# Kernel optimization log

Measured on AMD Instinct MI355X. Metric: run time of the kernel, lower is better.

Reference implementation:

```python
import jax, jax.numpy as jnp
import numpy as np
from jax import lax

# ---- static config (mirrors cfg) ----
ACT_SIZE = 768
GROUP_SIZES = [2048, 2048, 4096, 8192, 16384]
DICT_SIZE = sum(GROUP_SIZES)            # 32768
GROUP_IDX = np.concatenate([[0], np.cumsum(GROUP_SIZES)]).tolist()
TOP_K = 32
TOP_K_AUX = 512
L1_COEFF = 0.0003
AUX_PENALTY = 0.03125
N_DEAD = 5.0
THRESH_LR = 0.01
BATCH = 2048


def setup_inputs() -> dict:
    key = jax.random.key(0)
    k1, k2, k3, k4 = jax.random.split(key, 4)
    x = jax.random.normal(k1, (BATCH, ACT_SIZE), dtype=jnp.float32)
    W_enc = jax.random.normal(k2, (ACT_SIZE, DICT_SIZE), dtype=jnp.float32) * 0.02
    W_dec = jax.random.normal(k3, (DICT_SIZE, ACT_SIZE), dtype=jnp.float32)
    W_dec = W_dec / jnp.linalg.norm(W_dec, axis=-1, keepdims=True)  # unit-norm rows as in __init__
    num_batches_not_active = jax.random.randint(k4, (DICT_SIZE,), 0, 10).astype(jnp.float32)
    threshold = jnp.float32(0.0)
    return {"x": x, "W_enc": W_enc, "W_dec": W_dec, "b_dec": jnp.zeros((ACT_SIZE,), jnp.float32),
            "num_batches_not_active": num_batches_not_active, "threshold": threshold}


def reference(x, W_enc, W_dec, b_dec, num_batches_not_active, threshold):
    B, D = x.shape[0], DICT_SIZE
    # ---- preprocess (input_unit_norm=True) ----
    x_mean = x.mean(axis=-1, keepdims=True)
    x_std = jnp.std(x, axis=-1, keepdims=True, ddof=1)  # torch .std is unbiased
    xn = (x - x_mean) / (x_std + 1e-5)

    x_cent = xn - b_dec
    # ---- encode + global batch top-k (training path) ----
    acts = jax.nn.relu(x_cent @ W_enc)                  # [B, D]
    flat = acts.reshape(-1)
    k = TOP_K * B
    vals, idx = lax.top_k(flat, k)
    acts_topk = jnp.zeros_like(flat).at[idx].set(vals).reshape(B, D)

    # threshold EMA update (no_grad in torch)
    atk = lax.stop_gradient(acts_topk)
    pos = atk > 0
    min_pos = jnp.min(jnp.where(pos, atk, jnp.inf))
    new_threshold = jnp.where(pos.any(), (1 - THRESH_LR) * threshold + THRESH_LR * min_pos, threshold)

    # ---- matryoshka group decode ----
    x_reconstruct = jnp.broadcast_to(b_dec, xn.shape)
    inters = []
    for i in range(len(GROUP_SIZES)):
        s, e = GROUP_IDX[i], GROUP_IDX[i + 1]
        x_reconstruct = acts_topk[:, s:e] @ W_dec[s:e, :] + x_reconstruct
        inters.append(x_reconstruct)

    # ---- inactive-feature bookkeeping (no_grad) ----
    col_sums = lax.stop_gradient(acts_topk).sum(axis=0)
    nb = jnp.where(col_sums > 0, 0.0, num_batches_not_active + 1.0)

    # ---- loss dict ----
    total_l2 = jnp.mean((b_dec - xn) ** 2)
    l2s = jnp.stack([jnp.mean((r - xn) ** 2) for r in inters])
    total_l2 = total_l2 + l2s.sum()
    mean_l2 = total_l2 / (len(inters) + 1)
    x_var = jnp.var(xn, ddof=1)
    fvu = mean_l2 / (x_var + 1e-10)
    l1_norm = jnp.abs(acts_topk).sum(-1).mean()
    l0_norm = (acts_topk > 0).astype(jnp.float32).sum(-1).mean()
    l1_loss = L1_COEFF * l1_norm

    # ---- auxiliary loss over dead features ----
    dead = nb >= N_DEAD                                  # [D] bool, static count >> TOP_K_AUX here
    residual = xn - x_reconstruct
    masked = jnp.where(dead[None, :], acts, -jnp.inf)    # restrict top-k to dead features
    vals_a, idx_a = lax.top_k(masked, TOP_K_AUX)         # per-row top-k, [B, TOP_K_AUX]
    vals_a = jnp.where(jnp.isfinite(vals_a), vals_a, 0.0)
    acts_aux = jnp.zeros((B, D), acts.dtype).at[jnp.arange(B)[:, None], idx_a].set(vals_a)
    aux_reconstruct = acts_aux @ W_dec
    aux_mse = jnp.mean((aux_reconstruct - residual) ** 2)
    aux_loss = jnp.where(jnp.abs(aux_reconstruct).sum() > 0, AUX_PENALTY * aux_mse, 0.0)

    loss = mean_l2 + l1_loss + aux_loss
    num_dead_features = (nb > N_DEAD).sum()
    sae_out = x_reconstruct * x_std + x_mean

    return (sae_out, acts_topk, loss, l1_loss, mean_l2, l2s.min(), l2s.max(),
            l0_norm, l1_norm, aux_loss, new_threshold, fvu, num_dead_features)
```

## Files before the change

### kernel.cpp

```cpp
#include <hip/hip_runtime.h>
#include <stdint.h>

#define DEVFN static __device__ __forceinline__

typedef unsigned short u16;
typedef unsigned long long u64;
typedef short short8 __attribute__((ext_vector_type(8)));
typedef float vf4 __attribute__((ext_vector_type(4)));

constexpr int B = 2048;
constexpr int DIN = 768;
constexpr int D = 32768;
constexpr int NDI = B * D;
constexpr unsigned TOPK_TOTAL = 65536u;
constexpr int TOPK_AUX = 512;
constexpr int ROWCAP = 512;
constexpr int CANDCAP = 3145728;
constexpr int GSTAGE = 2048;
constexpr int CSTAGE = 4096;
constexpr int TIECAP = 4096;
constexpr int SCAP = 3072;
constexpr int NREP = 16;

constexpr size_t OFF_HIST1  = 0;
constexpr size_t OFF_HIST2  = 131072;
constexpr size_t OFF_HIST3  = 262144;
constexpr size_t OFF_HIST4  = 393216;
constexpr size_t OFF_SCALU  = 458752;
constexpr size_t OFF_SCALD  = 459008;
constexpr size_t OFF_ROWCNT = 459264;
constexpr size_t OFF_AUXCNT = 467456;
constexpr size_t OFF_COLACT = 475648;
constexpr size_t ZERO_BYTES = 606720;
constexpr size_t OFF_XN    = ZERO_BYTES;
constexpr size_t OFF_RES   = OFF_XN   + 6291456;
constexpr size_t OFF_RMEAN = OFF_RES  + 6291456;
constexpr size_t OFF_RSTD  = OFF_RMEAN + 8192;
constexpr size_t OFF_XNCB  = OFF_RSTD + 8192;
constexpr size_t OFF_DEAD  = OFF_XNCB + 3145728;
constexpr size_t OFF_DMASK = OFF_DEAD + 131072;
constexpr size_t OFF_DBASE = OFF_DMASK + 4096;
constexpr size_t OFF_RLC   = OFF_DBASE + 2048;
constexpr size_t OFF_RLV   = OFF_RLC  + 4194304;
constexpr size_t OFF_AXC   = OFF_RLV  + 4194304;
constexpr size_t OFF_AXV   = OFF_AXC  + 4194304;
constexpr size_t OFF_CANDI = OFF_AXV  + 4194304;
constexpr size_t OFF_CANDV = OFF_CANDI + (size_t)CANDCAP * 4;
constexpr size_t OFF_TIEB  = OFF_CANDV + (size_t)CANDCAP * 4;
constexpr size_t OFF_WT    = OFF_TIEB + (size_t)TIECAP * 4;


DEVFN u16 f2bf(float f) {
  unsigned u = __float_as_uint(f);
  unsigned r = (u + 0x7FFFu + ((u >> 16) & 1u)) >> 16;
  return (u16)r;
}
DEVFN float b2f(u16 h) { return __uint_as_float(((unsigned)h) << 16); }

DEVFN float bsumf(float v, float* red) {
  int t = threadIdx.x;
  red[t] = v; __syncthreads();
  for (int o = 128; o > 0; o >>= 1) { if (t < o) red[t] += red[t + o]; __syncthreads(); }
  float r = red[0]; __syncthreads();
  return r;
}
DEVFN unsigned bsumu(unsigned v, unsigned* red) {
  int t = threadIdx.x;
  red[t] = v; __syncthreads();
  for (int o = 128; o > 0; o >>= 1) { if (t < o) red[t] += red[t + o]; __syncthreads(); }
  unsigned r = red[0]; __syncthreads();
  return r;
}

DEVFN void findBin(const unsigned* hist, int nb, unsigned K, unsigned base,
                   unsigned* sscan, int* s_b, unsigned* s_cnt)
{
  int t = threadIdx.x;
  int chunk = nb >> 8;
  int hi = nb - 1 - t * chunk;
  unsigned p = 0;
  for (int k = 0; k < chunk; ++k) p += hist[hi - k];
  sscan[t] = p; __syncthreads();
  for (int o = 1; o < 256; o <<= 1) {
    unsigned xx = (t >= o) ? sscan[t - o] : 0u; __syncthreads();
    sscan[t] += xx; __syncthreads();
  }
  unsigned incl = sscan[t], excl = incl - p;
  unsigned cum = base + excl;
  if (base + incl >= K && cum < K) {
    unsigned acc = cum;
    for (int k = 0; k < chunk; ++k) {
      unsigned h = hist[hi - k];
      if (acc + h >= K) { *s_b = hi - k; *s_cnt = acc; break; }
      acc += h;
    }
  }
  __syncthreads();
}

__global__ __launch_bounds__(256) void k_rowstats(
    const float* __restrict__ x, const float* __restrict__ bdec,
    float* __restrict__ xn, u16* __restrict__ xncb,
    float* __restrict__ rmean, float* __restrict__ rstd, double* scalD)
{
  __shared__ float red[256];
  const int row = blockIdx.x, t = threadIdx.x;
  const float* xr = x + (size_t)row * DIN;
  float v0 = xr[t], v1 = xr[t + 256], v2 = xr[t + 512];
  float mean = bsumf(v0 + v1 + v2, red) * (1.0f / DIN);
  float d0 = v0 - mean, d1 = v1 - mean, d2 = v2 - mean;
  float var = bsumf(d0 * d0 + d1 * d1 + d2 * d2, red) * (1.0f / (DIN - 1));
  float sd = sqrtf(var);
  float inv = 1.0f / (sd + 1e-5f);
  float n0 = d0 * inv, n1 = d1 * inv, n2 = d2 * inv;
  size_t o = (size_t)row * DIN;
  xn[o + t] = n0; xn[o + t + 256] = n1; xn[o + t + 512] = n2;
  float b0 = bdec[t], b1 = bdec[t + 256], b2 = bdec[t + 512];
  xncb[o + t] = f2bf(n0 - b0); xncb[o + t + 256] = f2bf(n1 - b1); xncb[o + t + 512] = f2bf(n2 - b2);
  if (t == 0) { rmean[row] = mean; rstd[row] = sd; }
  float sxn = bsumf(n0 + n1 + n2, red);
  float ssq = bsumf(n0 * n0 + n1 * n1 + n2 * n2, red);
  float e0 = b0 - n0, e1 = b1 - n1, e2 = b2 - n2;
  float sq0 = bsumf(e0 * e0 + e1 * e1 + e2 * e2, red);
  if (t == 0) {
    atomicAdd(&scalD[1], (double)sxn);
    atomicAdd(&scalD[2], (double)ssq);
    atomicAdd(&scalD[3], (double)sq0);
  }
}

__global__ __launch_bounds__(256) void k_wt(const float* __restrict__ W, u16* __restrict__ Wt)
{
  __shared__ float tl[64][65];
  const int t = threadIdx.x;
  const int n0 = blockIdx.x * 64, k0 = blockIdx.y * 64;
  const int rr = t >> 6, cc = t & 63;
#pragma unroll
  for (int r = 0; r < 16; ++r) {
    int kk = r * 4 + rr;
    tl[kk][cc] = W[(size_t)(k0 + kk) * D + n0 + cc];
  }
  __syncthreads();
#pragma unroll
  for (int r = 0; r < 16; ++r) {
    int nn = r * 4 + rr;
    Wt[(size_t)(n0 + nn) * DIN + k0 + cc] = f2bf(tl[cc][nn]);
  }
}

__global__ __launch_bounds__(256) void k_wdecb(const float4* __restrict__ W4, u16* __restrict__ Wb)
{
  int stride = gridDim.x * blockDim.x;
  const int n4 = (D * DIN) / 4;
  for (int i = blockIdx.x * 256 + threadIdx.x; i < n4; i += stride) {
    float4 f = W4[i];
    unsigned p0 = (unsigned)f2bf(f.x) | ((unsigned)f2bf(f.y) << 16);
    unsigned p1 = (unsigned)f2bf(f.z) | ((unsigned)f2bf(f.w) << 16);
    uint2 q; q.x = p0; q.y = p1;
    *(uint2*)&Wb[(size_t)i * 4] = q;
  }
}

__global__ __launch_bounds__(256) void k_gemm(const u16* __restrict__ A,
                                              const u16* __restrict__ Bt,
                                              float* __restrict__ C,
                                              unsigned* __restrict__ hist16,
                                              unsigned* __restrict__ scalU,
                                              unsigned* __restrict__ candI,
                                              float* __restrict__ candV)
{
  __shared__ __align__(16) char lds[32768];
  __shared__ unsigned sCnt, sBase;
  const int tid = threadIdx.x, lane = tid & 63, wid = tid >> 6;
  const int bm = blockIdx.x * 128, bn = blockIdx.y * 128;

  const char* pA[4]; const char* pB[4];
#pragma unroll
  for (int i = 0; i < 4; ++i) {
    int G = i * 256 + wid * 64 + lane;
    int r = G >> 3, c = (G & 7) ^ (r & 7);
    pA[i] = (const char*)(A + (size_t)(bm + r) * DIN + c * 8);
    pB[i] = (const char*)(Bt + (size_t)(bn + r) * DIN + c * 8);
  }
  int aoff[2][4], boff[2][4];
#pragma unroll
  for (int kc = 0; kc < 2; ++kc)
#pragma unroll
    for (int i = 0; i < 4; ++i) {
      int cs = kc * 4 + (lane >> 4);
      int rA = (wid >> 1) * 64 + i * 16 + (lane & 15);
      aoff[kc][i] = rA * 128 + ((cs ^ (rA & 7)) * 16);
      int rB = (wid & 1) * 64 + i * 16 + (lane & 15);
      boff[kc][i] = 16384 + rB * 128 + ((cs ^ (rB & 7)) * 16);
    }

  vf4 acc[4][4];
#pragma unroll
  for (int i = 0; i < 4; ++i)
#pragma unroll
    for (int j = 0; j < 4; ++j) acc[i][j] = (vf4)0.f;

  for (int ks = 0; ks < 12; ++ks) {
    __syncthreads();
#pragma unroll
    for (int i = 0; i < 4; ++i) {
      __builtin_amdgcn_global_load_lds(
          (const __attribute__((address_space(1))) void*)pA[i],
          (__attribute__((address_space(3))) void*)(lds + (i * 256 + wid * 64) * 16), 16, 0, 0);
      __builtin_amdgcn_global_load_lds(
          (const __attribute__((address_space(1))) void*)pB[i],
          (__attribute__((address_space(3))) void*)(lds + 16384 + (i * 256 + wid * 64) * 16), 16, 0, 0);
      pA[i] += 128; pB[i] += 128;
    }
    __syncthreads();
#pragma unroll
    for (int kc = 0; kc < 2; ++kc) {
      short8 av[4], bv[4];
#pragma unroll
      for (int i = 0; i < 4; ++i) {
        av[i] = *(const short8*)(lds + aoff[kc][i]);
        bv[i] = *(const short8*)(lds + boff[kc][i]);
      }
#pragma unroll
      for (int i = 0; i < 4; ++i)
#pragma unroll
        for (int j = 0; j < 4; ++j)
          acc[i][j] = __builtin_amdgcn_mfma_f32_16x16x32_bf16(av[i], bv[j], acc[i][j], 0, 0, 0);
    }
  }

  unsigned* h = (unsigned*)lds;
  unsigned* stIdx = (unsigned*)(lds + 8192);
  float* stVal = (float*)(lds + 16384);
  __syncthreads();
  for (int j = tid; j < 2048; j += 256) h[j] = 0;
  if (tid == 0) sCnt = 0;
  __syncthreads();

  const int r0 = bm + (wid >> 1) * 64 + (lane >> 4) * 4;
  const int c0 = bn + (wid & 1) * 64 + (lane & 15);
#pragma unroll
  for (int i = 0; i < 4; ++i)
#pragma unroll
    for (int j = 0; j < 4; ++j) {
      float* cp = C + (size_t)(r0 + i * 16) * D + c0 + j * 16;
#pragma unroll
      for (int q = 0; q < 4; ++q) {
        float v = fmaxf(acc[i][j][q], 0.f);
        cp[(size_t)q * D] = v;
        if (v >= 1.0f) {
          atomicAdd(&h[__float_as_uint(v) >> 21], 1u);
          unsigned idx = ((unsigned)(r0 + i * 16 + q) << 15) | (unsigned)(c0 + j * 16);
          unsigned p = atomicAdd(&sCnt, 1u);
          if (p < (unsigned)GSTAGE) { stIdx[p] = idx; stVal[p] = v; }
          else {
            unsigned g = atomicAdd(&scalU[12], 1u);
            if (g < (unsigned)CANDCAP) { candI[g] = idx; candV[g] = v; }
          }
        }
      }
    }
  __syncthreads();
  unsigned* dst = hist16 + (size_t)(blockIdx.x & (NREP - 1)) * 2048;
  for (int j = 508 + tid; j < 2048; j += 256) {
    unsigned c = h[j];
    if (c) atomicAdd(&dst[j], c);
  }
  unsigned n = sCnt < (unsigned)GSTAGE ? sCnt : (unsigned)GSTAGE;
  if (tid == 0) sBase = atomicAdd(&scalU[12], n);
  __syncthreads();
  unsigned base = sBase;
  for (unsigned jj = tid; jj < n; jj += 256) {
    unsigned g = base + jj;
    if (g < (unsigned)CANDCAP) { candI[g] = stIdx[jj]; candV[g] = stVal[jj]; }
  }
}

__global__ __launch_bounds__(256) void k_scan1a(unsigned* scalU, const unsigned* __restrict__ h16)
{
  __shared__ unsigned hsum[2048];
  __shared__ unsigned sscan[256];
  __shared__ int s_b; __shared__ unsigned s_cnt;
  int t = threadIdx.x;
  for (int j = t; j < 2048; j += 256) {
    unsigned s = 0;
#pragma unroll
    for (int r = 0; r < NREP; ++r) s += h16[r * 2048 + j];
    hsum[j] = s;
  }
  if (t == 0) { s_b = 0; s_cnt = 0; }
  __syncthreads();
  unsigned p = 0;
  for (int j = 508 + t; j < 2048; j += 256) p += hsum[j];
  unsigned total = bsumu(p, sscan);
  if (total >= TOPK_TOTAL) {
    findBin(hsum, 2048, TOPK_TOTAL, 0u, sscan, &s_b, &s_cnt);
    if (t == 0) { scalU[0] = (unsigned)s_b; scalU[1] = s_cnt; scalU[13] = 0u; }
  } else if (t == 0) { scalU[13] = 1u; scalU[12] = 0u; }
}

__global__ __launch_bounds__(256) void k_histfull(const float4* __restrict__ a4,
    const unsigned* __restrict__ scalU, unsigned* __restrict__ h16)
{
  if (scalU[13] == 0u) return;
  __shared__ unsigned lh[4][2048];
  for (int j = threadIdx.x; j < 8192; j += 256) ((unsigned*)lh)[j] = 0;
  __syncthreads();
  unsigned* mylh = lh[threadIdx.x & 3];
  int stride = gridDim.x * blockDim.x;
  for (int i = blockIdx.x * 256 + threadIdx.x; i < NDI / 4; i += stride) {
    float4 f = a4[i];
    if (f.x > 0.f) atomicAdd(&mylh[__float_as_uint(f.x) >> 21], 1u);
    if (f.y > 0.f) atomicAdd(&mylh[__float_as_uint(f.y) >> 21], 1u);
    if (f.z > 0.f) atomicAdd(&mylh[__float_as_uint(f.z) >> 21], 1u);
    if (f.w > 0.f) atomicAdd(&mylh[__float_as_uint(f.w) >> 21], 1u);
  }
  __syncthreads();
  unsigned* dst = h16 + (size_t)(blockIdx.x & (NREP - 1)) * 2048;
  for (int j = threadIdx.x; j < 2048; j += 256) {
    unsigned c = lh[0][j] + lh[1][j] + lh[2][j] + lh[3][j];
    if (c) atomicAdd(&dst[j], c);
  }
}

__global__ __launch_bounds__(256) void k_scan1b(unsigned* scalU, const unsigned* __restrict__ h16)
{
  if (scalU[13] == 0u) return;
  __shared__ unsigned hsum[2048];
  __shared__ unsigned sscan[256];
  __shared__ int s_b; __shared__ unsigned s_cnt;
  int t = threadIdx.x;
  for (int j = t; j < 2048; j += 256) {
    unsigned s = 0;
#pragma unroll
    for (int r = 0; r < NREP; ++r) s += h16[r * 2048 + j];
    hsum[j] = s;
  }
  if (t == 0) { s_b = 0; s_cnt = 0; }
  __syncthreads();
  findBin(hsum, 2048, TOPK_TOTAL, 0u, sscan, &s_b, &s_cnt);
  if (t == 0) { scalU[0] = (unsigned)s_b; scalU[1] = s_cnt; }
}

__global__ __launch_bounds__(256) void k_compact(const float4* __restrict__ a4,
    unsigned* scalU, unsigned* __restrict__ candI, float* __restrict__ candV)
{
  if (scalU[13] == 0u) return;
  __shared__ unsigned sIdx[CSTAGE];
  __shared__ float sVal[CSTAGE];
  __shared__ unsigned sCnt, sBase;
  if (threadIdx.x == 0) sCnt = 0;
  __syncthreads();
  unsigned b1 = scalU[0];
  int stride = gridDim.x * blockDim.x;
  for (int i = blockIdx.x * 256 + threadIdx.x; i < NDI / 4; i += stride) {
    float4 f = a4[i];
    float vv[4] = {f.x, f.y, f.z, f.w};
#pragma unroll
    for (int c = 0; c < 4; ++c) {
      float v = vv[c];
      if (v > 0.f && (__float_as_uint(v) >> 21) >= b1) {
        unsigned p = atomicAdd(&sCnt, 1u);
        if (p < (unsigned)CSTAGE) { sIdx[p] = (unsigned)(i * 4 + c); sVal[p] = v; }
        else {
          unsigned g = atomicAdd(&scalU[12], 1u);
          if (g < (unsigned)CANDCAP) { candI[g] = (unsigned)(i * 4 + c); candV[g] = v; }
        }
      }
    }
  }
  __syncthreads();
  unsigned n = sCnt < (unsigned)CSTAGE ? sCnt : (unsigned)CSTAGE;
  if (threadIdx.x == 0) sBase = atomicAdd(&scalU[12], n);
  __syncthreads();
  unsigned base = sBase;
  for (unsigned j = threadIdx.x; j < n; j += 256) {
    unsigned g = base + j;
    if (g < (unsigned)CANDCAP) { candI[g] = sIdx[j]; candV[g] = sVal[j]; }
  }
}

__global__ __launch_bounds__(256) void k_rhist2(const unsigned* __restrict__ scalU,
    const float* __restrict__ candV, unsigned* __restrict__ h16)
{
  __shared__ unsigned lh[2048];
  for (int j = threadIdx.x; j < 2048; j += 256) lh[j] = 0;
  __syncthreads();
  unsigned b1 = scalU[0];
  int n = (int)scalU[12]; if (n > CANDCAP) n = CANDCAP;
  int stride = gridDim.x * blockDim.x;
  for (int j = blockIdx.x * 256 + threadIdx.x; j < n; j += stride) {
    unsigned u = __float_as_uint(candV[j]);
    if ((u >> 21) == b1) atomicAdd(&lh[(u >> 10) & 0x7FFu], 1u);
  }
  __syncthreads();
  unsigned* dst = h16 + (size_t)(blockIdx.x & (NREP - 1)) * 2048;
  for (int j = threadIdx.x; j < 2048; j += 256) {
    unsigned c = lh[j];
    if (c) atomicAdd(&dst[j], c);
  }
}

__global__ __launch_bounds__(256) void k_rscan2(unsigned* scalU, const unsigned* __restrict__ h16)
{
  __shared__ unsigned hsum[2048];
  __shared__ unsigned sscan[256];
  __shared__ int s_b; __shared__ unsigned s_cnt;
  int t = threadIdx.x;
  for (int j = t; j < 2048; j += 256) {
    unsigned s = 0;
#pragma unroll
    for (int r = 0; r < NREP; ++r) s += h16[r * 2048 + j];
    hsum[j] = s;
  }
  if (t == 0) { s_b = 0; s_cnt = 0; }
  __syncthreads();
  findBin(hsum, 2048, TOPK_TOTAL, scalU[1], sscan, &s_b, &s_cnt);
  if (t == 0) { scalU[2] = (unsigned)s_b; scalU[3] = s_cnt; }
}

__global__ __launch_bounds__(256) void k_rhist3(const unsigned* __restrict__ scalU,
    const float* __restrict__ candV, unsigned* __restrict__ h16)
{
  __shared__ unsigned lh[1024];
  for (int j = threadIdx.x; j < 1024; j += 256) lh[j] = 0;
  __syncthreads();
  unsigned b1 = scalU[0], b2 = scalU[2];
  int n = (int)scalU[12]; if (n > CANDCAP) n = CANDCAP;
  int stride = gridDim.x * blockDim.x;
  for (int j = blockIdx.x * 256 + threadIdx.x; j < n; j += stride) {
    unsigned u = __float_as_uint(candV[j]);
    if ((u >> 21) == b1 && ((u >> 10) & 0x7FFu) == b2) atomicAdd(&lh[u & 0x3FFu], 1u);
  }
  __syncthreads();
  unsigned* dst = h16 + (size_t)(blockIdx.x & (NREP - 1)) * 1024;
  for (int j = threadIdx.x; j < 1024; j += 256) {
    unsigned c = lh[j];
    if (c) atomicAdd(&dst[j], c);
  }
}

__global__ __launch_bounds__(256) void k_rscan3(unsigned* scalU, const unsigned* __restrict__ h16)
{
  __shared__ unsigned hsum[1024];
  __shared__ unsigned sscan[256];
  __shared__ int s_b; __shared__ unsigned s_cnt;
  int t = threadIdx.x;
  for (int j = t; j < 1024; j += 256) {
    unsigned s = 0;
#pragma unroll
    for (int r = 0; r < NREP; ++r) s += h16[r * 1024 + j];
    hsum[j] = s;
  }
  if (t == 0) { s_b = 0; s_cnt = 0; }
  __syncthreads();
  findBin(hsum, 1024, TOPK_TOTAL, scalU[3], sscan, &s_b, &s_cnt);
  if (t == 0) {
    unsigned cut = (scalU[0] << 21) | (scalU[2] << 10) | (unsigned)s_b;
    scalU[4] = cut; scalU[5] = s_cnt; scalU[6] = TOPK_TOTAL - s_cnt;
  }
}

__global__ __launch_bounds__(256) void k_tiecol(unsigned* scalU,
    const unsigned* __restrict__ candI, const float* __restrict__ candV,
    unsigned* __restrict__ tieB)
{
  unsigned cut = scalU[4];
  int n = (int)scalU[12]; if (n > CANDCAP) n = CANDCAP;
  int stride = gridDim.x * blockDim.x;
  for (int j = blockIdx.x * 256 + threadIdx.x; j < n; j += stride) {
    if (__float_as_uint(candV[j]) == cut) {
      unsigned p = atomicAdd(&scalU[14], 1u);
      if (p < (unsigned)TIECAP) tieB[p] = candI[j];
    }
  }
}

__global__ __launch_bounds__(256) void k_tieres(unsigned* scalU, const unsigned* __restrict__ tieB)
{
  __shared__ unsigned tbuf[TIECAP];
  __shared__ int sthr;
  int t = threadIdx.x;
  int m = (int)scalU[14]; if (m > TIECAP) m = TIECAP;
  int need = (int)scalU[6];
  for (int j = t; j < m; j += 256) tbuf[j] = tieB[j];
  if (t == 0) sthr = 0x7FFFFFFF;
  __syncthreads();
  if (need < m) {
    for (int ci = t; ci < m; ci += 256) {
      unsigned me = tbuf[ci];
      int r = 0;
      for (int j = 0; j < m; ++j) r += (tbuf[j] < me) ? 1 : 0;
      if (r == need - 1) sthr = (int)me;
    }
  }
  __syncthreads();
  if (t == 0) scalU[7] = (unsigned)sthr;
}

__global__ __launch_bounds__(256) void k_s1b(unsigned* scalU,
    const unsigned* __restrict__ candI, const float* __restrict__ candV,
    unsigned* rowCnt, unsigned* rlc, float* rlv, unsigned* colAct, double* scalD)
{
  __shared__ float redf[256];
  __shared__ unsigned redu[256];
  unsigned cut = scalU[4]; int tthr = (int)scalU[7];
  int n = (int)scalU[12]; if (n > CANDCAP) n = CANDCAP;
  float l1 = 0.f; unsigned l0 = 0;
  int stride = gridDim.x * blockDim.x;
  for (int j = blockIdx.x * 256 + threadIdx.x; j < n; j += stride) {
    float v = candV[j];
    unsigned u = __float_as_uint(v);
    unsigned idx = candI[j];
    if (u > cut || (u == cut && (int)idx <= tthr)) {
      int row = (int)(idx >> 15), col = (int)(idx & (D - 1));
      unsigned slot = atomicAdd(&rowCnt[row], 1u);
      if (slot < ROWCAP) {
        rlc[(size_t)row * ROWCAP + slot] = (unsigned)col;
        rlv[(size_t)row * ROWCAP + slot] = v;
      }
      colAct[col] = 1u;
      l1 += v; l0++;
    }
  }
  float l1s = bsumf(l1, redf);
  unsigned l0s = bsumu(l0, redu);
  if (threadIdx.x == 0) { atomicAdd(&scalD[0], (double)l1s); atomicAdd(&scalU[9], l0s); }
}

__global__ __launch_bounds__(256) void k_scatter(const unsigned* __restrict__ scalU,
    const unsigned* __restrict__ candI, const float* __restrict__ candV, float* __restrict__ acts)
{
  unsigned cut = scalU[4]; int tthr = (int)scalU[7];
  int n = (int)scalU[12]; if (n > CANDCAP) n = CANDCAP;
  int stride = gridDim.x * blockDim.x;
  for (int j = blockIdx.x * 256 + threadIdx.x; j < n; j += stride) {
    float v = candV[j];
    unsigned u = __float_as_uint(v);
    unsigned idx = candI[j];
    if (u > cut || (u == cut && (int)idx <= tthr)) acts[idx] = v;
  }
}

__global__ __launch_bounds__(256) void k_dead(const unsigned* __restrict__ colAct,
    const float* __restrict__ nbna, unsigned* deadCols, unsigned* scalU,
    u64* __restrict__ dmask, unsigned* __restrict__ dbase)
{
  __shared__ unsigned scan[256];
  __shared__ unsigned svd;
  const int t = threadIdx.x;
  if (t == 0) svd = 0;
  __syncthreads();
  const int c0 = t * 128;
  u64 w0 = 0, w1 = 0;
  unsigned vd = 0;
  for (int i = 0; i < 64; ++i) {
    int c = c0 + i;
    bool act = colAct[c] != 0;
    float f = nbna[c] + 1.0f;
    if (!act && f >= 5.0f) w0 |= (1ull << i);
    vd += (!act && f > 5.0f) ? 1u : 0u;
  }
  for (int i = 0; i < 64; ++i) {
    int c = c0 + 64 + i;
    bool act = colAct[c] != 0;
    float f = nbna[c] + 1.0f;
    if (!act && f >= 5.0f) w1 |= (1ull << i);
    vd += (!act && f > 5.0f) ? 1u : 0u;
  }
  unsigned cnt = (unsigned)(__popcll(w0) + __popcll(w1));
  scan[t] = cnt; __syncthreads();
  for (int o = 1; o < 256; o <<= 1) {
    unsigned xx = (t >= o) ? scan[t - o] : 0u; __syncthreads();
    scan[t] += xx; __syncthreads();
  }
  unsigned p = scan[t] - cnt;
  dmask[2 * t] = w0; dmask[2 * t + 1] = w1;
  dbase[2 * t] = p; dbase[2 * t + 1] = p + (unsigned)__popcll(w0);
  atomicAdd(&svd, vd);
  __syncthreads();
  if (t == 255) scalU[10] = scan[255];
  if (t == 0) scalU[11] = svd;
  (void)deadCols;
}

__global__ __launch_bounds__(256) void k_auxsel(const float* __restrict__ acts,
    const unsigned* __restrict__ scalU, const u64* __restrict__ dmask,
    unsigned* auxC, float* auxV, unsigned* auxN)
{
  __shared__ u64 smask[512];
  __shared__ unsigned hist[2048];
  __shared__ unsigned sscan[256];
  __shared__ float tval[SCAP];
  __shared__ unsigned tcol[SCAP];
  __shared__ int s_b; __shared__ unsigned s_cnt;
  __shared__ unsigned s_sel, s_tm;
  const int row = blockIdx.x, t = threadIdx.x;
  const float4* arow4 = (const float4*)(acts + (size_t)row * D);

  for (int j = t; j < 512; j += 256) smask[j] = dmask[j];
  for (int j = t; j < 2048; j += 256) hist[j] = 0;
  if (t == 0) { s_sel = 0; s_tm = 0; s_b = 0; s_cnt = 0; }
  __syncthreads();

  unsigned pcnt = 0;
  for (int j = t; j < D / 4; j += 256) {
    float4 f = arow4[j];
    u64 w = smask[j >> 4];
    int sh = (j & 15) * 4;
    float vv[4] = {f.x, f.y, f.z, f.w};
#pragma unroll
    for (int c = 0; c < 4; ++c) {
      if (((w >> (sh + c)) & 1ull) && vv[c] > 0.f) {
        pcnt++;
        atomicAdd(&hist[__float_as_uint(vv[c]) >> 21], 1u);
      }
    }
  }
  unsigned P = bsumu(pcnt, sscan);
  unsigned* outC = auxC + (size_t)row * TOPK_AUX;
  float* outV = auxV + (size_t)row * TOPK_AUX;

  if (P <= (unsigned)TOPK_AUX) {
    for (int j = t; j < D / 4; j += 256) {
      float4 f = arow4[j];
      u64 w = smask[j >> 4];
      int sh = (j & 15) * 4;
      float vv[4] = {f.x, f.y, f.z, f.w};
#pragma unroll
      for (int c = 0; c < 4; ++c)
        if (((w >> (sh + c)) & 1ull) && vv[c] > 0.f) {
          unsigned s = atomicAdd(&s_sel, 1u);
          outC[s] = (unsigned)(j * 4 + c); outV[s] = vv[c];
        }
    }
    __syncthreads();
    if (t == 0) auxN[row] = s_sel;
    return;
  }

  __syncthreads();
  findBin(hist, 2048, (unsigned)TOPK_AUX, 0u, sscan, &s_b, &s_cnt);
  unsigned b1 = (unsigned)s_b, c1 = s_cnt;

  for (int j = t; j < D / 4; j += 256) {
    float4 f = arow4[j];
    u64 w = smask[j >> 4];
    int sh = (j & 15) * 4;
    float vv[4] = {f.x, f.y, f.z, f.w};
#pragma unroll
    for (int c = 0; c < 4; ++c) {
      if (((w >> (sh + c)) & 1ull) && vv[c] > 0.f) {
        unsigned bin = __float_as_uint(vv[c]) >> 21;
        if (bin > b1) {
          unsigned s = atomicAdd(&s_sel, 1u);
          outC[s] = (unsigned)(j * 4 + c); outV[s] = vv[c];
        } else if (bin == b1) {
          unsigned p = atomicAdd(&s_tm, 1u);
          if (p < (unsigned)SCAP) { tcol[p] = (unsigned)(j * 4 + c); tval[p] = vv[c]; }
        }
      }
    }
  }
  __syncthreads();
  int m = (int)s_tm;

  if (m <= SCAP) {
    for (int j = t; j < 2048; j += 256) hist[j] = 0;
    if (t == 0) { s_b = 0; s_cnt = 0; }
    __syncthreads();
    for (int j = t; j < m; j += 256)
      atomicAdd(&hist[(__float_as_uint(tval[j]) >> 10) & 0x7FFu], 1u);
    __syncthreads();
    findBin(hist, 2048, (unsigned)TOPK_AUX, c1, sscan, &s_b, &s_cnt);
    unsigned b2 = (unsigned)s_b, c2 = s_cnt;
    for (int j = t; j < 1024; j += 256) hist[j] = 0;
    if (t == 0) { s_b = 0; s_cnt = 0; }
    __syncthreads();
    for (int j = t; j < m; j += 256) {
      unsigned u = __float_as_uint(tval[j]);
      if (((u >> 10) & 0x7FFu) == b2) atomicAdd(&hist[u & 0x3FFu], 1u);
    }
    __syncthreads();
    findBin(hist, 1024, (unsigned)TOPK_AUX, c2, sscan, &s_b, &s_cnt);
    unsigned cut = (b1 << 21) | (b2 << 10) | (unsigned)s_b;
    int need = TOPK_AUX - (int)s_cnt;
    for (int j = t; j < m; j += 256) {
      unsigned u = __float_as_uint(tval[j]);
      if (u > cut) {
        unsigned s = atomicAdd(&s_sel, 1u);
        outC[s] = tcol[j]; outV[s] = tval[j];
      } else if (u == cut) {
        unsigned col = tcol[j];
        int r = 0;
        for (int k = 0; k < m; ++k)
          r += (__float_as_uint(tval[k]) == cut && tcol[k] < col) ? 1 : 0;
        if (r < need) { unsigned s = atomicAdd(&s_sel, 1u); outC[s] = col; outV[s] = tval[j]; }
      }
    }
    __syncthreads();
    if (t == 0) auxN[row] = s_sel;
    return;
  }

  for (int j = t; j < 2048; j += 256) hist[j] = 0;
  if (t == 0) { s_b = 0; s_cnt = 0; }
  __syncthreads();
  for (int j = t; j < D / 4; j += 256) {
    float4 f = arow4[j];
    u64 w = smask[j >> 4];
    int sh = (j & 15) * 4;
    float vv[4] = {f.x, f.y, f.z, f.w};
#pragma unroll
    for (int c = 0; c < 4; ++c) {
      if (((w >> (sh + c)) & 1ull) && vv[c] > 0.f) {
        unsigned u = __float_as_uint(vv[c]);
        if ((u >> 21) == b1) atomicAdd(&hist[(u >> 10) & 0x7FFu], 1u);
      }
    }
  }
  __syncthreads();
  findBin(hist, 2048, (unsigned)TOPK_AUX, c1, sscan, &s_b, &s_cnt);
  unsigned b2 = (unsigned)s_b, c2 = s_cnt;
  for (int j = t; j < 1024; j += 256) hist[j] = 0;
  if (t == 0) { s_b = 0; s_cnt = 0; }
  __syncthreads();
  unsigned hi21 = (b1 << 11) | b2;
  for (int j = t; j < D / 4; j += 256) {
    float4 f = arow4[j];
    u64 w = smask[j >> 4];
    int sh = (j & 15) * 4;
    float vv[4] = {f.x, f.y, f.z, f.w};
#pragma unroll
    for (int c = 0; c < 4; ++c) {
      if (((w >> (sh + c)) & 1ull) && vv[c] > 0.f) {
        unsigned u = __float_as_uint(vv[c]);
        if ((u >> 10) == hi21) atomicAdd(&hist[u & 0x3FFu], 1u);
      }
    }
  }
  __syncthreads();
  findBin(hist, 1024, (unsigned)TOPK_AUX, c2, sscan, &s_b, &s_cnt);
  unsigned cut = (b1 << 21) | (b2 << 10) | (unsigned)s_b;
  int need = TOPK_AUX - (int)s_cnt;
  if (t == 0) s_tm = 0;
  __syncthreads();
  for (int j = t; j < D / 4; j += 256) {
    float4 f = arow4[j];
    u64 w = smask[j >> 4];
    int sh = (j & 15) * 4;
    float vv[4] = {f.x, f.y, f.z, f.w};
#pragma unroll
    for (int c = 0; c < 4; ++c) {
      if (((w >> (sh + c)) & 1ull) && vv[c] > 0.f) {
        unsigned u = __float_as_uint(vv[c]);
        if (u > cut && (u >> 21) == b1) {
          unsigned s = atomicAdd(&s_sel, 1u);
          outC[s] = (unsigned)(j * 4 + c); outV[s] = vv[c];
        } else if (u == cut) {
          unsigned p = atomicAdd(&s_tm, 1u);
          if (p < (unsigned)SCAP) tcol[p] = (unsigned)(j * 4 + c);
        }
      }
    }
  }
  __syncthreads();
  int mm = (int)s_tm; if (mm > SCAP) mm = SCAP;
  float cv = __uint_as_float(cut);
  for (int ci = t; ci < mm; ci += 256) {
    unsigned col = tcol[ci];
    int r = 0;
    for (int j = 0; j < mm; ++j) r += (tcol[j] < col) ? 1 : 0;
    if (r < need) { unsigned s = atomicAdd(&s_sel, 1u); outC[s] = col; outV[s] = cv; }
  }
  __syncthreads();
  if (t == 0) auxN[row] = s_sel;
}

__global__ __launch_bounds__(256) void k_decode(const u16* __restrict__ Wdecb,
    const float* __restrict__ bdec, const float* __restrict__ xn,
    const unsigned* __restrict__ rowCnt, const unsigned* __restrict__ rlc,
    const float* __restrict__ rlv, const float* __restrict__ rmean,
    const float* __restrict__ rstd, float* __restrict__ sae,
    float* __restrict__ resid, double* scalD)
{
  __shared__ int tlc[ROWCAP]; __shared__ float tlv[ROWCAP];
  __shared__ int slc[ROWCAP]; __shared__ float slv[ROWCAP];
  __shared__ int gcnt[5], gpos[5], gend[5];
  __shared__ float red[256];
  const int row = blockIdx.x, t = threadIdx.x;
  int cnt = (int)rowCnt[row]; if (cnt > ROWCAP) cnt = ROWCAP;
  if (t < 5) gcnt[t] = 0;
  __syncthreads();
  for (int e = t; e < cnt; e += 256) {
    int c = (int)rlc[(size_t)row * ROWCAP + e];
    tlc[e] = c; tlv[e] = rlv[(size_t)row * ROWCAP + e];
    int ilog = 31 - __clz(c | 1);
    int g = ilog > 10 ? ilog - 10 : 0;
    atomicAdd(&gcnt[g], 1);
  }
  __syncthreads();
  if (t == 0) {
    int b = 0;
    for (int g = 0; g < 5; ++g) { gpos[g] = b; b += gcnt[g]; gend[g] = b; }
  }
  __syncthreads();
  for (int e = t; e < cnt; e += 256) {
    int c = tlc[e];
    int ilog = 31 - __clz(c | 1);
    int g = ilog > 10 ? ilog - 10 : 0;
    int p = atomicAdd(&gpos[g], 1);
    slc[p] = c; slv[p] = tlv[e];
  }
  __syncthreads();
  float r0 = bdec[t], r1 = bdec[t + 256], r2 = bdec[t + 512];
  size_t o = (size_t)row * DIN;
  float x0 = xn[o + t], x1 = xn[o + t + 256], x2 = xn[o + t + 512];
  int e = 0;
#pragma unroll 1
  for (int g = 0; g < 5; ++g) {
    int e1 = gend[g];
#pragma unroll 2
    for (; e < e1; ++e) {
      int c = slc[e]; float v = slv[e];
      const u16* w = Wdecb + (size_t)c * DIN;
      r0 = fmaf(v, b2f(w[t]), r0);
      r1 = fmaf(v, b2f(w[t + 256]), r1);
      r2 = fmaf(v, b2f(w[t + 512]), r2);
    }
    float dd0 = r0 - x0, dd1 = r1 - x1, dd2 = r2 - x2;
    float sq = bsumf(dd0 * dd0 + dd1 * dd1 + dd2 * dd2, red);
    if (t == 0) atomicAdd(&scalD[4 + g], (double)sq);
  }
  float m = rmean[row], sd = rstd[row];
  sae[o + t] = r0 * sd + m; sae[o + t + 256] = r1 * sd + m; sae[o + t + 512] = r2 * sd + m;
  resid[o + t] = x0 - r0; resid[o + t + 256] = x1 - r1; resid[o + t + 512] = x2 - r2;
}

__global__ __launch_bounds__(256) void k_auxdec(const u16* __restrict__ Wdecb,
    const unsigned* __restrict__ auxC, const float* __restrict__ auxV,
    const unsigned* __restrict__ auxN, const float* __restrict__ resid, double* scalD)
{
  __shared__ int lc[TOPK_AUX]; __shared__ float lv[TOPK_AUX];
  __shared__ float red[256];
  const int row = blockIdx.x, t = threadIdx.x;
  int cnt = (int)auxN[row]; if (cnt > TOPK_AUX) cnt = TOPK_AUX;
  for (int e = t; e < cnt; e += 256) {
    lc[e] = (int)auxC[(size_t)row * TOPK_AUX + e];
    lv[e] = auxV[(size_t)row * TOPK_AUX + e];
  }
  __syncthreads();
  float a0 = 0.f, a1 = 0.f, a2 = 0.f;
#pragma unroll 4
  for (int e = 0; e < cnt; ++e) {
    int c = lc[e]; float v = lv[e];
    const u16* w = Wdecb + (size_t)c * DIN;
    a0 = fmaf(v, b2f(w[t]), a0);
    a1 = fmaf(v, b2f(w[t + 256]), a1);
    a2 = fmaf(v, b2f(w[t + 512]), a2);
  }
  size_t o = (size_t)row * DIN;
  float s0 = resid[o + t], s1 = resid[o + t + 256], s2 = resid[o + t + 512];
  float d0 = a0 - s0, d1 = a1 - s1, d2 = a2 - s2;
  float sq = bsumf(d0 * d0 + d1 * d1 + d2 * d2, red);
  float ab = bsumf(fabsf(a0) + fabsf(a1) + fabsf(a2), red);
  if (t == 0) { atomicAdd(&scalD[9], (double)sq); atomicAdd(&scalD[10], (double)ab); }
}

__global__ void k_final(const unsigned* __restrict__ scalU, const double* __restrict__ scalD,
                        const float* __restrict__ thr, float* __restrict__ out)
{
  if (threadIdx.x != 0 || blockIdx.x != 0) return;
  const double NEL = (double)B * (double)DIN;
  double term0 = scalD[3] / NEL;
  double tot = term0;
  double mn = 1e300, mx = -1e300;
  for (int g = 0; g < 5; ++g) {
    double l2 = scalD[4 + g] / NEL;
    tot += l2;
    mn = l2 < mn ? l2 : mn;
    mx = l2 > mx ? l2 : mx;
  }
  double mean_l2 = tot / 6.0;
  double sum = scalD[1], ssq = scalD[2];
  double xvar = (ssq - sum * sum / NEL) / (NEL - 1.0);
  double fvu = mean_l2 / (xvar + 1e-10);
  double l1n = scalD[0] / (double)B;
  double l1loss = (double)0.0003f * l1n;
  double l0n = (double)scalU[9] / (double)B;
  double auxmse = scalD[9] / NEL;
  double auxloss = (scalD[10] > 0.0) ? 0.03125 * auxmse : 0.0;
  double loss = mean_l2 + l1loss + auxloss;
  float cutv = __uint_as_float(scalU[4]);
  float t0 = thr[0];
  float newthr = (scalU[9] > 0u) ? (0.99f * t0 + 0.01f * cutv) : t0;
  float* s = out + (size_t)B * DIN + (size_t)NDI;
  s[0] = (float)loss;   s[1] = (float)l1loss; s[2] = (float)mean_l2;
  s[3] = (float)mn;     s[4] = (float)mx;     s[5] = (float)l0n;
  s[6] = (float)l1n;    s[7] = (float)auxloss; s[8] = newthr;
  s[9] = (float)fvu;    s[10] = (float)scalU[11];
}

extern "C" void kernel_launch(void* const* d_in, const int* in_sizes, int n_in,
                              void* d_out, int out_size, void* d_ws, size_t ws_size,
                              hipStream_t stream)
{
  (void)in_sizes; (void)n_in; (void)out_size; (void)ws_size;
  const float* x    = (const float*)d_in[0];
  const float* Wenc = (const float*)d_in[1];
  const float* Wdec = (const float*)d_in[2];
  const float* bdec = (const float*)d_in[3];
  const float* nbna = (const float*)d_in[4];
  const float* thr  = (const float*)d_in[5];
  float* out = (float*)d_out;
  char* ws = (char*)d_ws;

  float* sae  = out;
  float* acts = out + (size_t)B * DIN;

  unsigned* hist1 = (unsigned*)(ws + OFF_HIST1);
  unsigned* hist2 = (unsigned*)(ws + OFF_HIST2);
  unsigned* hist3 = (unsigned*)(ws + OFF_HIST3);
  unsigned* hist4 = (unsigned*)(ws + OFF_HIST4);
  unsigned* scalU = (unsigned*)(ws + OFF_SCALU);
  double*   scalD = (double*)(ws + OFF_SCALD);
  unsigned* rowCnt= (unsigned*)(ws + OFF_ROWCNT);
  unsigned* auxN  = (unsigned*)(ws + OFF_AUXCNT);
  unsigned* colAct= (unsigned*)(ws + OFF_COLACT);
  float* xn    = (float*)(ws + OFF_XN);
  float* resid = (float*)(ws + OFF_RES);
  float* rmean = (float*)(ws + OFF_RMEAN);
  float* rstd  = (float*)(ws + OFF_RSTD);
  u16*   xncb  = (u16*)(ws + OFF_XNCB);
  unsigned* deadC = (unsigned*)(ws + OFF_DEAD);
  u64*      dmask = (u64*)(ws + OFF_DMASK);
  unsigned* dbase = (unsigned*)(ws + OFF_DBASE);
  unsigned* rlc = (unsigned*)(ws + OFF_RLC);
  float*    rlv = (float*)(ws + OFF_RLV);
  unsigned* auxC = (unsigned*)(ws + OFF_AXC);
  float*    auxV = (float*)(ws + OFF_AXV);
  unsigned* candI = (unsigned*)(ws + OFF_CANDI);
  float*    candV = (float*)(ws + OFF_CANDV);
  unsigned* tieB  = (unsigned*)(ws + OFF_TIEB);
  u16* Wt    = (u16*)(ws + OFF_WT);
  u16* Wdecb = (u16*)(ws + OFF_WT);

  hipMemsetAsync(ws, 0, ZERO_BYTES, stream);
  hipLaunchKernelGGL(k_rowstats, dim3(B), dim3(256), 0, stream, x, bdec, xn, xncb, rmean, rstd, scalD);
  hipLaunchKernelGGL(k_wt, dim3(D / 64, DIN / 64), dim3(256), 0, stream, Wenc, Wt);
  hipLaunchKernelGGL(k_gemm, dim3(B / 128, D / 128), dim3(256), 0, stream, xncb, Wt, acts, hist1, scalU, candI, candV);
  hipLaunchKernelGGL(k_scan1a, dim3(1), dim3(256), 0, stream, scalU, hist1);
  hipLaunchKernelGGL(k_histfull, dim3(2048), dim3(256), 0, stream, (const float4*)acts, scalU, hist2);
  hipLaunchKernelGGL(k_scan1b, dim3(1), dim3(256), 0, stream, scalU, hist2);
  hipLaunchKernelGGL(k_compact, dim3(2048), dim3(256), 0, stream, (const float4*)acts, scalU, candI, candV);
  hipLaunchKernelGGL(k_wdecb, dim3(2048), dim3(256), 0, stream, (const float4*)Wdec, Wdecb);
  hipLaunchKernelGGL(k_rhist2, dim3(256), dim3(256), 0, stream, scalU, candV, hist3);
  hipLaunchKernelGGL(k_rscan2, dim3(1), dim3(256), 0, stream, scalU, hist3);
  hipLaunchKernelGGL(k_rhist3, dim3(256), dim3(256), 0, stream, scalU, candV, hist4);
  hipLaunchKernelGGL(k_rscan3, dim3(1), dim3(256), 0, stream, scalU, hist4);
  hipLaunchKernelGGL(k_tiecol, dim3(256), dim3(256), 0, stream, scalU, candI, candV, tieB);
  hipLaunchKernelGGL(k_tieres, dim3(1), dim3(256), 0, stream, scalU, tieB);
  hipLaunchKernelGGL(k_s1b, dim3(256), dim3(256), 0, stream, scalU, candI, candV, rowCnt, rlc, rlv, colAct, scalD);
  hipLaunchKernelGGL(k_dead, dim3(1), dim3(256), 0, stream, colAct, nbna, deadC, scalU, dmask, dbase);
  hipLaunchKernelGGL(k_auxsel, dim3(B), dim3(256), 0, stream, acts, scalU, dmask, auxC, auxV, auxN);
  hipMemsetAsync(acts, 0, (size_t)NDI * 4, stream);
  hipLaunchKernelGGL(k_scatter, dim3(256), dim3(256), 0, stream, scalU, candI, candV, acts);
  hipLaunchKernelGGL(k_decode, dim3(B), dim3(256), 0, stream, Wdecb, bdec, xn, rowCnt, rlc, rlv, rmean, rstd, sae, resid, scalD);
  hipLaunchKernelGGL(k_auxdec, dim3(B), dim3(256), 0, stream, Wdecb, auxC, auxV, auxN, resid, scalD);
  hipLaunchKernelGGL(k_final, dim3(1), dim3(64), 0, stream, scalU, scalD, thr, out);
}
```

Before: 977.7 us.

## Store dense activations as bf16 scratch and aggregate candidate atomics per wavefront

```diff
diff --git a/kernel.cpp b/kernel.cpp
--- a/kernel.cpp
+++ b/kernel.cpp
@@ -163,7 +163,7 @@
 
 __global__ __launch_bounds__(256) void k_gemm(const u16* __restrict__ A,
                                               const u16* __restrict__ Bt,
-                                              float* __restrict__ C,
+                                              u16* __restrict__ Cb,
                                               unsigned* __restrict__ hist16,
                                               unsigned* __restrict__ scalU,
                                               unsigned* __restrict__ candI,
@@ -172,7 +172,7 @@
   __shared__ __align__(16) char lds[32768];
   __shared__ unsigned sCnt, sBase;
   const int tid = threadIdx.x, lane = tid & 63, wid = tid >> 6;
-  const int bm = blockIdx.x * 128, bn = blockIdx.y * 128;
+  const int bn = blockIdx.x * 128, bm = blockIdx.y * 128;
 
   const char* pA[4]; const char* pB[4];
 #pragma unroll
@@ -243,19 +243,28 @@
   for (int i = 0; i < 4; ++i)
 #pragma unroll
     for (int j = 0; j < 4; ++j) {
-      float* cp = C + (size_t)(r0 + i * 16) * D + c0 + j * 16;
+      u16* cp = Cb + (size_t)(r0 + i * 16) * D + c0 + j * 16;
 #pragma unroll
       for (int q = 0; q < 4; ++q) {
         float v = fmaxf(acc[i][j][q], 0.f);
-        cp[(size_t)q * D] = v;
-        if (v >= 1.0f) {
-          atomicAdd(&h[__float_as_uint(v) >> 21], 1u);
-          unsigned idx = ((unsigned)(r0 + i * 16 + q) << 15) | (unsigned)(c0 + j * 16);
-          unsigned p = atomicAdd(&sCnt, 1u);
-          if (p < (unsigned)GSTAGE) { stIdx[p] = idx; stVal[p] = v; }
-          else {
-            unsigned g = atomicAdd(&scalU[12], 1u);
-            if (g < (unsigned)CANDCAP) { candI[g] = idx; candV[g] = v; }
+        cp[(size_t)q * D] = f2bf(v);
+        bool sel = (v >= 1.0f);
+        u64 m = __ballot(sel);
+        if (m) {
+          if (sel) atomicAdd(&h[__float_as_uint(v) >> 21], 1u);
+          unsigned cnt = (unsigned)__popcll(m);
+          int leader = (int)__builtin_ctzll(m);
+          unsigned base = 0;
+          if (lane == leader) base = atomicAdd(&sCnt, cnt);
+          base = __shfl(base, leader, 64);
+          if (sel) {
+            unsigned p = base + (unsigned)__popcll(m & ((1ull << lane) - 1ull));
+            unsigned idx = ((unsigned)(r0 + i * 16 + q) << 15) | (unsigned)(c0 + j * 16);
+            if (p < (unsigned)GSTAGE) { stIdx[p] = idx; stVal[p] = v; }
+            else {
+              unsigned g = atomicAdd(&scalU[12], 1u);
+              if (g < (unsigned)CANDCAP) { candI[g] = idx; candV[g] = v; }
+            }
           }
         }
       }
@@ -299,7 +308,7 @@
   } else if (t == 0) { scalU[13] = 1u; scalU[12] = 0u; }
 }
 
-__global__ __launch_bounds__(256) void k_histfull(const float4* __restrict__ a4,
+__global__ __launch_bounds__(256) void k_histfull(const uint4* __restrict__ a8,
     const unsigned* __restrict__ scalU, unsigned* __restrict__ h16)
 {
   if (scalU[13] == 0u) return;
@@ -308,12 +317,14 @@
   __syncthreads();
   unsigned* mylh = lh[threadIdx.x & 3];
   int stride = gridDim.x * blockDim.x;
-  for (int i = blockIdx.x * 256 + threadIdx.x; i < NDI / 4; i += stride) {
-    float4 f = a4[i];
-    if (f.x > 0.f) atomicAdd(&mylh[__float_as_uint(f.x) >> 21], 1u);
-    if (f.y > 0.f) atomicAdd(&mylh[__float_as_uint(f.y) >> 21], 1u);
-    if (f.z > 0.f) atomicAdd(&mylh[__float_as_uint(f.z) >> 21], 1u);
-    if (f.w > 0.f) atomicAdd(&mylh[__float_as_uint(f.w) >> 21], 1u);
+  for (int i = blockIdx.x * 256 + threadIdx.x; i < NDI / 8; i += stride) {
+    uint4 f = a8[i];
+    unsigned uu[4] = {f.x, f.y, f.z, f.w};
+#pragma unroll
+    for (int c = 0; c < 8; ++c) {
+      unsigned hb = (uu[c >> 1] >> ((c & 1) * 16)) & 0xFFFFu;
+      if (hb && !(hb & 0x8000u)) atomicAdd(&mylh[hb >> 5], 1u);
+    }
   }
   __syncthreads();
   unsigned* dst = h16 + (size_t)(blockIdx.x & (NREP - 1)) * 2048;
@@ -342,7 +353,7 @@
   if (t == 0) { scalU[0] = (unsigned)s_b; scalU[1] = s_cnt; }
 }
 
-__global__ __launch_bounds__(256) void k_compact(const float4* __restrict__ a4,
+__global__ __launch_bounds__(256) void k_compact(const uint4* __restrict__ a8,
     unsigned* scalU, unsigned* __restrict__ candI, float* __restrict__ candV)
 {
   if (scalU[13] == 0u) return;
@@ -353,18 +364,18 @@
   __syncthreads();
   unsigned b1 = scalU[0];
   int stride = gridDim.x * blockDim.x;
-  for (int i = blockIdx.x * 256 + threadIdx.x; i < NDI / 4; i += stride) {
-    float4 f = a4[i];
-    float vv[4] = {f.x, f.y, f.z, f.w};
-#pragma unroll
-    for (int c = 0; c < 4; ++c) {
-      float v = vv[c];
-      if (v > 0.f && (__float_as_uint(v) >> 21) >= b1) {
+  for (int i = blockIdx.x * 256 + threadIdx.x; i < NDI / 8; i += stride) {
+    uint4 f = a8[i];
+    unsigned uu[4] = {f.x, f.y, f.z, f.w};
+#pragma unroll
+    for (int c = 0; c < 8; ++c) {
+      unsigned hb = (uu[c >> 1] >> ((c & 1) * 16)) & 0xFFFFu;
+      if (hb && !(hb & 0x8000u) && (hb >> 5) >= b1) {
         unsigned p = atomicAdd(&sCnt, 1u);
-        if (p < (unsigned)CSTAGE) { sIdx[p] = (unsigned)(i * 4 + c); sVal[p] = v; }
+        if (p < (unsigned)CSTAGE) { sIdx[p] = (unsigned)(i * 8 + c); sVal[p] = b2f((u16)hb); }
         else {
           unsigned g = atomicAdd(&scalU[12], 1u);
-          if (g < (unsigned)CANDCAP) { candI[g] = (unsigned)(i * 4 + c); candV[g] = v; }
+          if (g < (unsigned)CANDCAP) { candI[g] = (unsigned)(i * 8 + c); candV[g] = b2f((u16)hb); }
         }
       }
     }
@@ -584,7 +595,7 @@
   (void)deadCols;
 }
 
-__global__ __launch_bounds__(256) void k_auxsel(const float* __restrict__ acts,
+__global__ __launch_bounds__(256) void k_auxsel(const u16* __restrict__ actsb,
     const unsigned* __restrict__ scalU, const u64* __restrict__ dmask,
     unsigned* auxC, float* auxV, unsigned* auxN)
 {
@@ -596,7 +607,7 @@
   __shared__ int s_b; __shared__ unsigned s_cnt;
   __shared__ unsigned s_sel, s_tm;
   const int row = blockIdx.x, t = threadIdx.x;
-  const float4* arow4 = (const float4*)(acts + (size_t)row * D);
+  const uint4* arow8 = (const uint4*)(actsb + (size_t)row * D);
 
   for (int j = t; j < 512; j += 256) smask[j] = dmask[j];
   for (int j = t; j < 2048; j += 256) hist[j] = 0;
@@ -604,16 +615,17 @@
   __syncthreads();
 
   unsigned pcnt = 0;
-  for (int j = t; j < D / 4; j += 256) {
-    float4 f = arow4[j];
-    u64 w = smask[j >> 4];
-    int sh = (j & 15) * 4;
-    float vv[4] = {f.x, f.y, f.z, f.w};
-#pragma unroll
-    for (int c = 0; c < 4; ++c) {
-      if (((w >> (sh + c)) & 1ull) && vv[c] > 0.f) {
+  for (int j = t; j < D / 8; j += 256) {
+    uint4 f = arow8[j];
+    u64 w = smask[j >> 3];
+    int sh = (j & 7) * 8;
+    unsigned uu[4] = {f.x, f.y, f.z, f.w};
+#pragma unroll
+    for (int c = 0; c < 8; ++c) {
+      unsigned hb = (uu[c >> 1] >> ((c & 1) * 16)) & 0xFFFFu;
+      if (((w >> (sh + c)) & 1ull) && hb && !(hb & 0x8000u)) {
         pcnt++;
-        atomicAdd(&hist[__float_as_uint(vv[c]) >> 21], 1u);
+        atomicAdd(&hist[hb >> 5], 1u);
       }
     }
   }
@@ -622,17 +634,19 @@
   float* outV = auxV + (size_t)row * TOPK_AUX;
 
   if (P <= (unsigned)TOPK_AUX) {
-    for (int j = t; j < D / 4; j += 256) {
-      float4 f = arow4[j];
-      u64 w = smask[j >> 4];
-      int sh = (j & 15) * 4;
-      float vv[4] = {f.x, f.y, f.z, f.w};
-#pragma unroll
-      for (int c = 0; c < 4; ++c)
-        if (((w >> (sh + c)) & 1ull) && vv[c] > 0.f) {
+    for (int j = t; j < D / 8; j += 256) {
+      uint4 f = arow8[j];
+      u64 w = smask[j >> 3];
+      int sh = (j & 7) * 8;
+      unsigned uu[4] = {f.x, f.y, f.z, f.w};
+#pragma unroll
+      for (int c = 0; c < 8; ++c) {
+        unsigned hb = (uu[c >> 1] >> ((c & 1) * 16)) & 0xFFFFu;
+        if (((w >> (sh + c)) & 1ull) && hb && !(hb & 0x8000u)) {
           unsigned s = atomicAdd(&s_sel, 1u);
-          outC[s] = (unsigned)(j * 4 + c); outV[s] = vv[c];
+          outC[s] = (unsigned)(j * 8 + c); outV[s] = b2f((u16)hb);
         }
+      }
     }
     __syncthreads();
     if (t == 0) auxN[row] = s_sel;
@@ -643,21 +657,22 @@
   findBin(hist, 2048, (unsigned)TOPK_AUX, 0u, sscan, &s_b, &s_cnt);
   unsigned b1 = (unsigned)s_b, c1 = s_cnt;
 
-  for (int j = t; j < D / 4; j += 256) {
-    float4 f = arow4[j];
-    u64 w = smask[j >> 4];
-    int sh = (j & 15) * 4;
-    float vv[4] = {f.x, f.y, f.z, f.w};
-#pragma unroll
-    for (int c = 0; c < 4; ++c) {
-      if (((w >> (sh + c)) & 1ull) && vv[c] > 0.f) {
-        unsigned bin = __float_as_uint(vv[c]) >> 21;
+  for (int j = t; j < D / 8; j += 256) {
+    uint4 f = arow8[j];
+    u64 w = smask[j >> 3];
+    int sh = (j & 7) * 8;
+    unsigned uu[4] = {f.x, f.y, f.z, f.w};
+#pragma unroll
+    for (int c = 0; c < 8; ++c) {
+      unsigned hb = (uu[c >> 1] >> ((c & 1) * 16)) & 0xFFFFu;
+      if (((w >> (sh + c)) & 1ull) && hb && !(hb & 0x8000u)) {
+        unsigned bin = hb >> 5;
         if (bin > b1) {
           unsigned s = atomicAdd(&s_sel, 1u);
-          outC[s] = (unsigned)(j * 4 + c); outV[s] = vv[c];
+          outC[s] = (unsigned)(j * 8 + c); outV[s] = b2f((u16)hb);
         } else if (bin == b1) {
           unsigned p = atomicAdd(&s_tm, 1u);
-          if (p < (unsigned)SCAP) { tcol[p] = (unsigned)(j * 4 + c); tval[p] = vv[c]; }
+          if (p < (unsigned)SCAP) { tcol[p] = (unsigned)(j * 8 + c); tval[p] = b2f((u16)hb); }
         }
       }
     }
@@ -706,60 +721,43 @@
   for (int j = t; j < 2048; j += 256) hist[j] = 0;
   if (t == 0) { s_b = 0; s_cnt = 0; }
   __syncthreads();
-  for (int j = t; j < D / 4; j += 256) {
-    float4 f = arow4[j];
-    u64 w = smask[j >> 4];
-    int sh = (j & 15) * 4;
-    float vv[4] = {f.x, f.y, f.z, f.w};
-#pragma unroll
-    for (int c = 0; c < 4; ++c) {
-      if (((w >> (sh + c)) & 1ull) && vv[c] > 0.f) {
-        unsigned u = __float_as_uint(vv[c]);
-        if ((u >> 21) == b1) atomicAdd(&hist[(u >> 10) & 0x7FFu], 1u);
+  for (int j = t; j < D / 8; j += 256) {
+    uint4 f = arow8[j];
+    u64 w = smask[j >> 3];
+    int sh = (j & 7) * 8;
+    unsigned uu[4] = {f.x, f.y, f.z, f.w};
+#pragma unroll
+    for (int c = 0; c < 8; ++c) {
+      unsigned hb = (uu[c >> 1] >> ((c & 1) * 16)) & 0xFFFFu;
+      if (((w >> (sh + c)) & 1ull) && hb && !(hb & 0x8000u)) {
+        if ((hb >> 5) == b1) atomicAdd(&hist[((hb << 16) >> 10) & 0x7FFu], 1u);
       }
     }
   }
   __syncthreads();
   findBin(hist, 2048, (unsigned)TOPK_AUX, c1, sscan, &s_b, &s_cnt);
   unsigned b2 = (unsigned)s_b, c2 = s_cnt;
-  for (int j = t; j < 1024; j += 256) hist[j] = 0;
-  if (t == 0) { s_b = 0; s_cnt = 0; }
-  __syncthreads();
-  unsigned hi21 = (b1 << 11) | b2;
-  for (int j = t; j < D / 4; j += 256) {
-    float4 f = arow4[j];
-    u64 w = smask[j >> 4];
-    int sh = (j & 15) * 4;
-    float vv[4] = {f.x, f.y, f.z, f.w};
-#pragma unroll
-    for (int c = 0; c < 4; ++c) {
-      if (((w >> (sh + c)) & 1ull) && vv[c] > 0.f) {
-        unsigned u = __float_as_uint(vv[c]);
-        if ((u >> 10) == hi21) atomicAdd(&hist[u & 0x3FFu], 1u);
-      }
-    }
-  }
-  __syncthreads();
-  findBin(hist, 1024, (unsigned)TOPK_AUX, c2, sscan, &s_b, &s_cnt);
-  unsigned cut = (b1 << 21) | (b2 << 10) | (unsigned)s_b;
-  int need = TOPK_AUX - (int)s_cnt;
+  __syncthreads();
+  unsigned cut = (b1 << 21) | (b2 << 10);
+  int need = TOPK_AUX - (int)c2;
   if (t == 0) s_tm = 0;
   __syncthreads();
-  for (int j = t; j < D / 4; j += 256) {
-    float4 f = arow4[j];
-    u64 w = smask[j >> 4];
-    int sh = (j & 15) * 4;
-    float vv[4] = {f.x, f.y, f.z, f.w};
-#pragma unroll
-    for (int c = 0; c < 4; ++c) {
-      if (((w >> (sh + c)) & 1ull) && vv[c] > 0.f) {
-        unsigned u = __float_as_uint(vv[c]);
-        if (u > cut && (u >> 21) == b1) {
+  for (int j = t; j < D / 8; j += 256) {
+    uint4 f = arow8[j];
+    u64 w = smask[j >> 3];
+    int sh = (j & 7) * 8;
+    unsigned uu[4] = {f.x, f.y, f.z, f.w};
+#pragma unroll
+    for (int c = 0; c < 8; ++c) {
+      unsigned hb = (uu[c >> 1] >> ((c & 1) * 16)) & 0xFFFFu;
+      if (((w >> (sh + c)) & 1ull) && hb && !(hb & 0x8000u)) {
+        unsigned u = hb << 16;
+        if (u > cut) {
           unsigned s = atomicAdd(&s_sel, 1u);
-          outC[s] = (unsigned)(j * 4 + c); outV[s] = vv[c];
+          outC[s] = (unsigned)(j * 8 + c); outV[s] = __uint_as_float(u);
         } else if (u == cut) {
           unsigned p = atomicAdd(&s_tm, 1u);
-          if (p < (unsigned)SCAP) tcol[p] = (unsigned)(j * 4 + c);
+          if (p < (unsigned)SCAP) tcol[p] = (unsigned)(j * 8 + c);
         }
       }
     }
@@ -917,6 +915,7 @@
 
   float* sae  = out;
   float* acts = out + (size_t)B * DIN;
+  u16*  actsb = (u16*)(out + (size_t)B * DIN);
 
   unsigned* hist1 = (unsigned*)(ws + OFF_HIST1);
   unsigned* hist2 = (unsigned*)(ws + OFF_HIST2);
@@ -948,11 +947,11 @@
   hipMemsetAsync(ws, 0, ZERO_BYTES, stream);
   hipLaunchKernelGGL(k_rowstats, dim3(B), dim3(256), 0, stream, x, bdec, xn, xncb, rmean, rstd, scalD);
   hipLaunchKernelGGL(k_wt, dim3(D / 64, DIN / 64), dim3(256), 0, stream, Wenc, Wt);
-  hipLaunchKernelGGL(k_gemm, dim3(B / 128, D / 128), dim3(256), 0, stream, xncb, Wt, acts, hist1, scalU, candI, candV);
+  hipLaunchKernelGGL(k_gemm, dim3(D / 128, B / 128), dim3(256), 0, stream, xncb, Wt, actsb, hist1, scalU, candI, candV);
   hipLaunchKernelGGL(k_scan1a, dim3(1), dim3(256), 0, stream, scalU, hist1);
-  hipLaunchKernelGGL(k_histfull, dim3(2048), dim3(256), 0, stream, (const float4*)acts, scalU, hist2);
+  hipLaunchKernelGGL(k_histfull, dim3(2048), dim3(256), 0, stream, (const uint4*)actsb, scalU, hist2);
   hipLaunchKernelGGL(k_scan1b, dim3(1), dim3(256), 0, stream, scalU, hist2);
-  hipLaunchKernelGGL(k_compact, dim3(2048), dim3(256), 0, stream, (const float4*)acts, scalU, candI, candV);
+  hipLaunchKernelGGL(k_compact, dim3(2048), dim3(256), 0, stream, (const uint4*)actsb, scalU, candI, candV);
   hipLaunchKernelGGL(k_wdecb, dim3(2048), dim3(256), 0, stream, (const float4*)Wdec, Wdecb);
   hipLaunchKernelGGL(k_rhist2, dim3(256), dim3(256), 0, stream, scalU, candV, hist3);
   hipLaunchKernelGGL(k_rscan2, dim3(1), dim3(256), 0, stream, scalU, hist3);
@@ -962,7 +961,7 @@
   hipLaunchKernelGGL(k_tieres, dim3(1), dim3(256), 0, stream, scalU, tieB);
   hipLaunchKernelGGL(k_s1b, dim3(256), dim3(256), 0, stream, scalU, candI, candV, rowCnt, rlc, rlv, colAct, scalD);
   hipLaunchKernelGGL(k_dead, dim3(1), dim3(256), 0, stream, colAct, nbna, deadC, scalU, dmask, dbase);
-  hipLaunchKernelGGL(k_auxsel, dim3(B), dim3(256), 0, stream, acts, scalU, dmask, auxC, auxV, auxN);
+  hipLaunchKernelGGL(k_auxsel, dim3(B), dim3(256), 0, stream, actsb, scalU, dmask, auxC, auxV, auxN);
   hipMemsetAsync(acts, 0, (size_t)NDI * 4, stream);
   hipLaunchKernelGGL(k_scatter, dim3(256), dim3(256), 0, stream, scalU, candI, candV, acts);
   hipLaunchKernelGGL(k_decode, dim3(B), dim3(256), 0, stream, Wdecb, bdec, xn, rowCnt, rlc, rlv, rmean, rstd, sae, resid, scalD);
```

New measurement: 968.1 us. Within noise of the previous version (-1.0%).
